# Kernel optimization log

Hardware: AMD Instinct MI355X
Metric: run time of the kernel (lower is better)

## Reference

```python
import jax, jax.numpy as jnp
import numpy as np

B, G, C = 256, 64, 128          # pictures, groups/picture, curves/group
N = B * G * C                    # 2,097,152 flat curves
EPS = 1e-5


def _bn(x, gamma, beta):
    # torch BatchNorm1d training-mode math: biased variance over batch dim
    mu = x.mean(axis=0)
    var = ((x - mu) ** 2).mean(axis=0)
    return (x - mu) / jnp.sqrt(var + EPS) * gamma + beta


def setup_inputs() -> dict:
    key = jax.random.key(0)
    ks = jax.random.split(key, 16)
    rn = lambda k, s: jax.random.normal(k, s, dtype=jnp.float32) * 0.1
    return {
        "x": jax.random.normal(ks[0], (N, 32), dtype=jnp.float32),
        "dist_mat": jax.random.normal(ks[1], (B, G, 2, 5), dtype=jnp.float32),
        "segment_ids": jnp.arange(N, dtype=jnp.int32) // C,  # curve -> group id
        "w1": rn(ks[2], (24, 32)), "b1": rn(ks[3], (24,)),
        "w2": rn(ks[4], (12, 24)), "b2": rn(ks[5], (12,)),
        "gamma12": jnp.ones((12,), jnp.float32), "beta12": jnp.zeros((12,), jnp.float32),
        "wd": rn(ks[6], (12, 5)), "bd": rn(ks[7], (12,)),
        "gamma36": jnp.ones((36,), jnp.float32), "beta36": jnp.zeros((36,), jnp.float32),
        "wp1": rn(ks[8], (18, 36)), "bp1": rn(ks[9], (18,)),
        "wp2": rn(ks[10], (8, 18)), "bp2": rn(ks[11], (8,)),
        "wp3": rn(ks[12], (2, 8)), "bp3": rn(ks[13], (2,)),
    }


def reference(x, dist_mat, segment_ids, w1, b1, w2, b2, gamma12, beta12,
              wd, bd, gamma36, beta36, wp1, bp1, wp2, bp2, wp3, bp3):
    leaky = jax.nn.leaky_relu  # slope 0.01, same as nn.LeakyReLU default
    # per-curve MLP: 32 -> 24 -> 12, then BatchNorm over all curves
    h = leaky(x @ w1.T + b1)               # [N, 24]
    h = leaky(h @ w2.T + b2)               # [N, 12]
    h = _bn(h, gamma12, beta12)            # [N, 12]
    # ragged segment-mean: curves -> groups (uniform segments of size C)
    groups = jax.ops.segment_sum(h, segment_ids, num_segments=B * G) / C
    groups = groups.reshape(B, G, 12)      # groups_layer1 per picture
    # distance adaptation: dist_mat[:, :, 0, :] -> Linear(5,12) -> leaky
    cor = leaky(jnp.einsum('bgk,dk->bgd', dist_mat[:, :, 0, :], wd) + bd)  # [B,G,12]
    # three pooling levels (distance-weighted elementwise-multiply reduce)
    L1 = groups.mean(axis=1)               # [B, 12]
    g2 = cor * groups
    L2 = g2.mean(axis=1)
    g3 = cor * g2
    L3 = g3.mean(axis=1)
    sum_pic = jnp.concatenate([L1, L2, L3], axis=1)  # [B, 36]
    s = _bn(sum_pic, gamma36, beta36)
    p1 = leaky(s @ wp1.T + bp1)            # [B, 18]
    p2 = leaky(p1 @ wp2.T + bp2)           # [B, 8]  (pred_level2)
    p3 = jax.nn.softmax(p2 @ wp3.T + bp3, axis=1)  # [B, 2] (pred_level3)
    return (p2, p3)
```

## Files before the change

### kernel.cpp

```cpp
#include <hip/hip_runtime.h>
#include <hip/hip_bf16.h>

#define N_CURVES 2097152
#define NG       16384
#define B_PIC    256
#define G_PER_B  64
#define NSLOT    64

__device__ __forceinline__ float leaky(float v) {
    return fmaxf(v, 0.01f * v);
}

__global__ __launch_bounds__(256, 4) void kA(const float* __restrict__ x,
                                             const float* __restrict__ w1,
                                             const float* __restrict__ b1,
                                             const float* __restrict__ w2,
                                             const float* __restrict__ b2,
                                             float* __restrict__ partials,
                                             float* __restrict__ groupSums)
{
    __shared__ float4 xs[256 * 8];
    __shared__ float wsum[4][12];
    __shared__ float wsq[4][12];

    const int tid = threadIdx.x;
    const size_t blockBase = (size_t)blockIdx.x * 2048;

    const float4* __restrict__ xg = (const float4*)x;
#pragma unroll
    for (int i = 0; i < 8; ++i) {
        const int idx = i * 256 + tid;
        const float4 v = xg[blockBase + idx];
        const int c = idx >> 3;
        const int j = idx & 7;
        xs[c * 8 + (j ^ (c & 7))] = v;
    }
    __syncthreads();

    float xr[32];
#pragma unroll
    for (int j = 0; j < 8; ++j) {
        const float4 v = xs[tid * 8 + (j ^ (tid & 7))];
        xr[4 * j + 0] = v.x; xr[4 * j + 1] = v.y;
        xr[4 * j + 2] = v.z; xr[4 * j + 3] = v.w;
    }

    float h1[24];
#pragma unroll
    for (int j = 0; j < 24; ++j) {
        float acc = b1[j];
#pragma unroll
        for (int k = 0; k < 32; ++k) acc = fmaf(xr[k], w1[j * 32 + k], acc);
        h1[j] = leaky(acc);
    }

    float h2[12];
#pragma unroll
    for (int j = 0; j < 12; ++j) {
        float acc = b2[j];
#pragma unroll
        for (int k = 0; k < 24; ++k) acc = fmaf(h1[k], w2[j * 24 + k], acc);
        h2[j] = leaky(acc);
    }

    const int lane = tid & 63, wid = tid >> 6;
#pragma unroll
    for (int c = 0; c < 12; ++c) {
        float v = h2[c];
        float q = v * v;
#pragma unroll
        for (int off = 32; off >= 1; off >>= 1) {
            v += __shfl_down(v, off);
            q += __shfl_down(q, off);
        }
        if (lane == 0) { wsum[wid][c] = v; wsq[wid][c] = q; }
    }
    __syncthreads();

    if (tid < 12) {
        const int c = tid;
        const float g0 = wsum[0][c] + wsum[1][c];
        const float g1 = wsum[2][c] + wsum[3][c];
        groupSums[(size_t)(2 * blockIdx.x) * 12 + c]     = g0;
        groupSums[(size_t)(2 * blockIdx.x + 1) * 12 + c] = g1;
        const int slot = blockIdx.x & (NSLOT - 1);
        atomicAdd(&partials[slot * 24 + c], g0 + g1);
        const float q = wsq[0][c] + wsq[1][c] + wsq[2][c] + wsq[3][c];
        atomicAdd(&partials[slot * 24 + 12 + c], q);
    }
}

__global__ __launch_bounds__(64) void kB(const float* __restrict__ partials,
                                         const float* __restrict__ groupSums,
                                         const float* __restrict__ dist,
                                         const float* __restrict__ wd,
                                         const float* __restrict__ bd,
                                         const float* __restrict__ gamma12,
                                         const float* __restrict__ beta12,
                                         float* __restrict__ sum_pic)
{
    __shared__ float scale[12], shift[12];
    const int g = threadIdx.x;
    const int b = blockIdx.x;

    if (g < 12) {
        float S = 0.f, Q = 0.f;
        for (int s = 0; s < NSLOT; ++s) {
            S += partials[s * 24 + g];
            Q += partials[s * 24 + 12 + g];
        }
        const float mu  = S * (1.0f / (float)N_CURVES);
        const float var = Q * (1.0f / (float)N_CURVES) - mu * mu;
        const float inv = rsqrtf(var + 1e-5f);
        scale[g] = inv * gamma12[g];
        shift[g] = beta12[g] - mu * inv * gamma12[g];
    }
    __syncthreads();

    const float* dm = dist + (size_t)(b * G_PER_B + g) * 2 * 5;
    const float d0 = dm[0], d1 = dm[1], d2 = dm[2], d3 = dm[3], d4 = dm[4];
    const float* gs = groupSums + (size_t)(b * G_PER_B + g) * 12;

    float a1[12], a2[12], a3[12];
#pragma unroll
    for (int d = 0; d < 12; ++d) {
        float cor = bd[d];
        cor = fmaf(d0, wd[d * 5 + 0], cor);
        cor = fmaf(d1, wd[d * 5 + 1], cor);
        cor = fmaf(d2, wd[d * 5 + 2], cor);
        cor = fmaf(d3, wd[d * 5 + 3], cor);
        cor = fmaf(d4, wd[d * 5 + 4], cor);
        cor = leaky(cor);
        float t = gs[d] * (1.0f / 128.0f);
        t = t * scale[d] + shift[d];
        a1[d] = t;
        a2[d] = cor * t;
        a3[d] = cor * cor * t;
    }

#pragma unroll
    for (int d = 0; d < 12; ++d) {
        float v1 = a1[d], v2 = a2[d], v3 = a3[d];
#pragma unroll
        for (int off = 32; off >= 1; off >>= 1) {
            v1 += __shfl_down(v1, off);
            v2 += __shfl_down(v2, off);
            v3 += __shfl_down(v3, off);
        }
        if (g == 0) {
            sum_pic[b * 36 + d]      = v1 * (1.0f / 64.0f);
            sum_pic[b * 36 + 12 + d] = v2 * (1.0f / 64.0f);
            sum_pic[b * 36 + 24 + d] = v3 * (1.0f / 64.0f);
        }
    }
}

__global__ __launch_bounds__(256) void kC(const float* __restrict__ sum_pic,
                                          const float* __restrict__ gamma36,
                                          const float* __restrict__ beta36,
                                          const float* __restrict__ wp1,
                                          const float* __restrict__ bp1,
                                          const float* __restrict__ wp2,
                                          const float* __restrict__ bp2,
                                          const float* __restrict__ wp3,
                                          const float* __restrict__ bp3,
                                          float* __restrict__ out)
{
    const int t = threadIdx.x;
    __shared__ float sm[256 * 37];
    __shared__ float scale[36], shift[36];

    float s[36];
#pragma unroll
    for (int c = 0; c < 36; ++c) {
        s[c] = sum_pic[t * 36 + c];
        sm[t * 37 + c] = s[c];
    }
    __syncthreads();

    if (t < 36) {
        float S = 0.f, Q = 0.f;
        for (int i = 0; i < 256; ++i) {
            const float v = sm[i * 37 + t];
            S += v;
            Q += v * v;
        }
        const float m   = S * (1.0f / 256.0f);
        const float inv = rsqrtf(Q * (1.0f / 256.0f) - m * m + 1e-5f);
        scale[t] = inv * gamma36[t];
        shift[t] = beta36[t] - m * inv * gamma36[t];
    }
    __syncthreads();

#pragma unroll
    for (int c = 0; c < 36; ++c)
        s[c] = s[c] * scale[c] + shift[c];

    float p1[18];
#pragma unroll
    for (int j = 0; j < 18; ++j) {
        float acc = bp1[j];
#pragma unroll
        for (int k = 0; k < 36; ++k) acc = fmaf(s[k], wp1[j * 36 + k], acc);
        p1[j] = leaky(acc);
    }
    float p2[8];
#pragma unroll
    for (int j = 0; j < 8; ++j) {
        float acc = bp2[j];
#pragma unroll
        for (int k = 0; k < 18; ++k) acc = fmaf(p1[k], wp2[j * 18 + k], acc);
        p2[j] = leaky(acc);
    }
    float l0 = bp3[0], l1 = bp3[1];
#pragma unroll
    for (int k = 0; k < 8; ++k) {
        l0 = fmaf(p2[k], wp3[k], l0);
        l1 = fmaf(p2[k], wp3[8 + k], l1);
    }
    const float m  = fmaxf(l0, l1);
    const float e0 = __expf(l0 - m);
    const float e1 = __expf(l1 - m);
    const float rd = 1.0f / (e0 + e1);

#pragma unroll
    for (int j = 0; j < 8; ++j) out[t * 8 + j] = p2[j];
    out[2048 + t * 2 + 0] = e0 * rd;
    out[2048 + t * 2 + 1] = e1 * rd;
}

extern "C" void kernel_launch(void* const* d_in, const int* in_sizes, int n_in,
                              void* d_out, int out_size, void* d_ws, size_t ws_size,
                              hipStream_t stream) {
    const float* x       = (const float*)d_in[0];
    const float* dist    = (const float*)d_in[1];
    const float* w1      = (const float*)d_in[3];
    const float* b1      = (const float*)d_in[4];
    const float* w2      = (const float*)d_in[5];
    const float* b2      = (const float*)d_in[6];
    const float* gamma12 = (const float*)d_in[7];
    const float* beta12  = (const float*)d_in[8];
    const float* wd      = (const float*)d_in[9];
    const float* bd      = (const float*)d_in[10];
    const float* gamma36 = (const float*)d_in[11];
    const float* beta36  = (const float*)d_in[12];
    const float* wp1     = (const float*)d_in[13];
    const float* bp1     = (const float*)d_in[14];
    const float* wp2     = (const float*)d_in[15];
    const float* bp2     = (const float*)d_in[16];
    const float* wp3     = (const float*)d_in[17];
    const float* bp3     = (const float*)d_in[18];

    float* ws        = (float*)d_ws;
    float* partials  = ws;
    float* groupSums = ws + NSLOT * 24;
    float* sum_pic   = groupSums + (size_t)NG * 12;

    hipMemsetAsync(partials, 0, NSLOT * 24 * sizeof(float), stream);

    kA<<<N_CURVES / 256, 256, 0, stream>>>(x, w1, b1, w2, b2, partials, groupSums);
    kB<<<B_PIC, G_PER_B, 0, stream>>>(partials, groupSums, dist, wd, bd,
                                      gamma12, beta12, sum_pic);
    kC<<<1, 256, 0, stream>>>(sum_pic, gamma36, beta36,
                              wp1, bp1, wp2, bp2, wp3, bp3, (float*)d_out);
}
```

Before: 445.0 us.

## Load x directly into LDS, fuse MLP layers, reduce via shared memory

Loads x tiles straight from global memory into LDS with the global_load_lds builtin, skipping the trip through registers, and keeps the XOR swizzle on the global address side. The two MLP layers are fused so each hidden unit is consumed right after it is computed, which removes the 24-element h1 array and lowers register pressure. The occupancy hint rises to 5 blocks per CU. The per-wave shuffle reduction is replaced by writing h2 into padded LDS and letting 24 threads serially sum 128 rows each, which trades shuffle work for a serial tail on a few threads.

```diff
diff --git a/kernel.cpp b/kernel.cpp
--- a/kernel.cpp
+++ b/kernel.cpp
@@ -11,7 +11,7 @@
     return fmaxf(v, 0.01f * v);
 }
 
-__global__ __launch_bounds__(256, 4) void kA(const float* __restrict__ x,
+__global__ __launch_bounds__(256, 5) void kA(const float* __restrict__ x,
                                              const float* __restrict__ w1,
                                              const float* __restrict__ b1,
                                              const float* __restrict__ w2,
@@ -19,21 +19,28 @@
                                              float* __restrict__ partials,
                                              float* __restrict__ groupSums)
 {
-    __shared__ float4 xs[256 * 8];
-    __shared__ float wsum[4][12];
-    __shared__ float wsq[4][12];
+    __shared__ __align__(16) char smem[32768];
+    float4* xs = (float4*)smem;
+    float*  sm = (float*)smem;
 
     const int tid = threadIdx.x;
     const size_t blockBase = (size_t)blockIdx.x * 2048;
-
     const float4* __restrict__ xg = (const float4*)x;
+
 #pragma unroll
     for (int i = 0; i < 8; ++i) {
-        const int idx = i * 256 + tid;
-        const float4 v = xg[blockBase + idx];
-        const int c = idx >> 3;
-        const int j = idx & 7;
-        xs[c * 8 + (j ^ (c & 7))] = v;
+        const int s  = i * 256 + tid;
+        const int c  = s >> 3;
+        const int j  = (s & 7) ^ (c & 7);
+        const float4* gp = xg + blockBase + c * 8 + j;
+        float4* lp = xs + (i * 256 + (tid & 192));
+#if defined(__has_builtin) && __has_builtin(__builtin_amdgcn_global_load_lds)
+        __builtin_amdgcn_global_load_lds(
+            (const __attribute__((address_space(1))) void*)gp,
+            (__attribute__((address_space(3))) void*)lp, 16, 0, 0);
+#else
+        xs[s] = *gp;
+#endif
     }
     __syncthreads();
 
@@ -44,49 +51,50 @@
         xr[4 * j + 0] = v.x; xr[4 * j + 1] = v.y;
         xr[4 * j + 2] = v.z; xr[4 * j + 3] = v.w;
     }
-
-    float h1[24];
+    __syncthreads();
+
+    float h2[12];
+#pragma unroll
+    for (int c = 0; c < 12; ++c) h2[c] = b2[c];
 #pragma unroll
     for (int j = 0; j < 24; ++j) {
-        float acc = b1[j];
-#pragma unroll
-        for (int k = 0; k < 32; ++k) acc = fmaf(xr[k], w1[j * 32 + k], acc);
-        h1[j] = leaky(acc);
-    }
-
-    float h2[12];
-#pragma unroll
-    for (int j = 0; j < 12; ++j) {
-        float acc = b2[j];
-#pragma unroll
-        for (int k = 0; k < 24; ++k) acc = fmaf(h1[k], w2[j * 24 + k], acc);
-        h2[j] = leaky(acc);
-    }
-
-    const int lane = tid & 63, wid = tid >> 6;
+        float t = b1[j];
+#pragma unroll
+        for (int k = 0; k < 32; ++k) t = fmaf(xr[k], w1[j * 32 + k], t);
+        t = leaky(t);
+#pragma unroll
+        for (int c = 0; c < 12; ++c) h2[c] = fmaf(t, w2[c * 24 + j], h2[c]);
+    }
 #pragma unroll
     for (int c = 0; c < 12; ++c) {
-        float v = h2[c];
-        float q = v * v;
-#pragma unroll
-        for (int off = 32; off >= 1; off >>= 1) {
-            v += __shfl_down(v, off);
-            q += __shfl_down(q, off);
-        }
-        if (lane == 0) { wsum[wid][c] = v; wsq[wid][c] = q; }
-    }
-    __syncthreads();
-
-    if (tid < 12) {
-        const int c = tid;
-        const float g0 = wsum[0][c] + wsum[1][c];
-        const float g1 = wsum[2][c] + wsum[3][c];
-        groupSums[(size_t)(2 * blockIdx.x) * 12 + c]     = g0;
-        groupSums[(size_t)(2 * blockIdx.x + 1) * 12 + c] = g1;
+        h2[c] = leaky(h2[c]);
+        sm[tid * 14 + c] = h2[c];
+    }
+    __syncthreads();
+
+    if (tid < 24) {
+        const int c = tid % 12;
+        const int g = tid / 12;
+        const float* base = sm + (size_t)g * 128 * 14 + c;
+        float S0 = 0.f, S1 = 0.f, S2 = 0.f, S3 = 0.f;
+        float Q0 = 0.f, Q1 = 0.f, Q2 = 0.f, Q3 = 0.f;
+#pragma unroll 8
+        for (int i = 0; i < 128; i += 4) {
+            const float v0 = base[(i + 0) * 14];
+            const float v1 = base[(i + 1) * 14];
+            const float v2 = base[(i + 2) * 14];
+            const float v3 = base[(i + 3) * 14];
+            S0 += v0; Q0 = fmaf(v0, v0, Q0);
+            S1 += v1; Q1 = fmaf(v1, v1, Q1);
+            S2 += v2; Q2 = fmaf(v2, v2, Q2);
+            S3 += v3; Q3 = fmaf(v3, v3, Q3);
+        }
+        const float S = (S0 + S1) + (S2 + S3);
+        const float Q = (Q0 + Q1) + (Q2 + Q3);
+        groupSums[(size_t)(2 * blockIdx.x + g) * 12 + c] = S;
         const int slot = blockIdx.x & (NSLOT - 1);
-        atomicAdd(&partials[slot * 24 + c], g0 + g1);
-        const float q = wsq[0][c] + wsq[1][c] + wsq[2][c] + wsq[3][c];
-        atomicAdd(&partials[slot * 24 + 12 + c], q);
+        atomicAdd(&partials[slot * 24 + c], S);
+        atomicAdd(&partials[slot * 24 + 12 + c], Q);
     }
 }
 
```

New measurement: 439.6 us. No clear change (-1.2%).
